# Kernel optimization log

Hardware: AMD Instinct MI355X
Metric: run time of the kernel (lower is better)

## Reference

```python
import jax, jax.numpy as jnp
import numpy as np

B, C, H, W = 4, 128, 64, 64


def setup_inputs() -> dict:
    key = jax.random.key(0)
    ks = jax.random.split(key, 4)
    x = jax.random.normal(ks[0], (B, C, H, W), dtype=jnp.float32)
    # 1x1 conv weights stored as [out_ch, in_ch]; biases [out_ch]
    Wf = jax.random.normal(ks[1], (1, C), dtype=jnp.float32) * 0.02
    bf = jnp.zeros((1,), dtype=jnp.float32)
    Wg = jax.random.normal(ks[2], (1, C), dtype=jnp.float32) * 0.02
    bg = jnp.zeros((1,), dtype=jnp.float32)
    Wh = jax.random.normal(ks[3], (C, C), dtype=jnp.float32) * 0.02
    bh = jnp.zeros((C,), dtype=jnp.float32)
    return {"x": x, "Wf": Wf, "bf": bf, "Wg": Wg, "bg": bg, "Wh": Wh, "bh": bh}


def reference(x, Wf, bf, Wg, bg, Wh, bh):
    b, c, h_, w_ = x.shape
    n = h_ * w_
    xf = x.reshape(b, c, n)  # [B, C, N]
    # 1x1 convs == per-pixel linear projections
    f = jnp.einsum('oc,bcn->bon', Wf, xf) + bf[None, :, None]  # [B, 1, N]
    g = jnp.einsum('oc,bcn->bon', Wg, xf) + bg[None, :, None]  # [B, 1, N]
    hh = jnp.einsum('oc,bcn->bon', Wh, xf) + bh[None, :, None]  # [B, C, N]
    # attention[b, i, j] = f[b, i] * g[b, j]; softmax over j (last dim)
    logits = jnp.einsum('bdi,bdj->bij', f, g)  # [B, N, N] (d=1)
    attn = jax.nn.softmax(logits, axis=-1)
    # bmm(h, attention): out[b, c, i] = sum_j h[b, c, j] * attn[b, j, i]
    sa = jnp.einsum('bcj,bji->bci', hh, attn)  # [B, C, N]
    return sa.reshape(b, c, h_, w_) + x
```

## Files before the change

kernel.cpp:

```cpp
#include <hip/hip_runtime.h>


#define B_ 4
#define C_ 128
#define N_ 4096
#define K_ 16

__device__ __forceinline__ float wave_reduce(float v) {
    #pragma unroll
    for (int off = 32; off > 0; off >>= 1) v += __shfl_down(v, off);
    return v;
}

__global__ __launch_bounds__(512) void kA(
    const float* __restrict__ x,
    const float* __restrict__ Wf, const float* __restrict__ bf,
    const float* __restrict__ Wg, const float* __restrict__ bg,
    float* __restrict__ f, float* __restrict__ g, float* __restrict__ Spart)
{
    int blk = blockIdx.x;
    int b   = blk >> 6;
    int n0  = (blk & 63) * 64;
    int tid = threadIdx.x, wave = tid >> 6, lane = tid & 63;

    const float* xb = x + (size_t)b * C_ * N_ + n0 + lane;
    float accf = 0.f, accg = 0.f;
    int cbeg = wave * 16;
    #pragma unroll
    for (int c = cbeg; c < cbeg + 16; ++c) {
        float xv = xb[(size_t)c * N_];
        accf += Wf[c] * xv;
        accg += Wg[c] * xv;
    }
    __shared__ float lf[8][64], lg[8][64];
    lf[wave][lane] = accf; lg[wave][lane] = accg;
    __syncthreads();
    if (tid < 64) {
        float s = 0.f;
        #pragma unroll
        for (int w2 = 0; w2 < 8; ++w2) s += lf[w2][tid];
        f[b * N_ + n0 + tid] = s + bf[0];
    } else if (tid < 128) {
        int l = lane;
        float s = 0.f;
        #pragma unroll
        for (int w2 = 0; w2 < 8; ++w2) s += lg[w2][l];
        float gv = s + bg[0];
        g[b * N_ + n0 + l] = gv;
        float p = 1.f;
        #pragma unroll
        for (int k = 0; k < K_; ++k) {
            float v = wave_reduce(p);
            if (l == 0) Spart[blk * K_ + k] = v;
            p *= gv;
        }
    }
}

__global__ __launch_bounds__(256) void kB(
    const float* __restrict__ x, const float* __restrict__ f,
    const float* __restrict__ Spart,
    float* __restrict__ Mt, float* __restrict__ t)
{
    static constexpr float INV_FACT[K_] = {
        1.f, 1.f, 0.5f, 1.6666667e-01f, 4.1666668e-02f, 8.3333338e-03f,
        1.3888889e-03f, 1.9841270e-04f, 2.4801587e-05f, 2.7557319e-06f,
        2.7557319e-07f, 2.5052108e-08f, 2.0876757e-09f, 1.6059044e-10f,
        1.1470746e-11f, 7.6471637e-13f };
    static constexpr float CK[K_] = {
        1.f, 0.5f, 3.3333334e-01f, 0.25f, 0.2f, 1.6666667e-01f,
        1.4285715e-01f, 0.125f, 1.1111111e-01f, 0.1f, 9.0909094e-02f,
        8.3333336e-02f, 7.6923079e-02f, 7.1428575e-02f, 6.6666670e-02f,
        6.25e-02f };

    int r   = blockIdx.x;
    int b   = r / (C_ + 1);
    int c   = r % (C_ + 1);
    int tid = threadIdx.x, wave = tid >> 6, lane = tid & 63;

    __shared__ float sred[16][16];
    __shared__ float Sfin[16];
    {
        int k = tid & 15, grp = tid >> 4;
        const float* Sp = Spart + (size_t)(b * 64 + grp * 4) * K_ + k;
        sred[grp][k] = Sp[0] + Sp[K_] + Sp[2 * K_] + Sp[3 * K_];
    }
    __syncthreads();
    if (tid < 16) {
        float s = 0.f;
        #pragma unroll
        for (int gi = 0; gi < 16; ++gi) s += sred[gi][tid];
        Sfin[tid] = s;
    }
    __syncthreads();
    float hk[K_];
    #pragma unroll
    for (int k = 0; k < K_; ++k) hk[k] = Sfin[k] * INV_FACT[k];

    const float* fb = f + b * N_;
    const float* xr = x + ((size_t)b * C_ + c) * N_;
    bool real = (c < C_);

    float acc[K_];
    #pragma unroll
    for (int k = 0; k < K_; ++k) acc[k] = 0.f;

    #pragma unroll
    for (int it = 0; it < 4; ++it) {
        int j = it * 1024 + tid * 4;
        float4 f4 = *(const float4*)(fb + j);
        float4 x4 = real ? *(const float4*)(xr + j) : make_float4(1.f, 1.f, 1.f, 1.f);
        float fe[4] = { f4.x, f4.y, f4.z, f4.w };
        float xe[4] = { x4.x, x4.y, x4.z, x4.w };
        #pragma unroll
        for (int e = 0; e < 4; ++e) {
            float fv = fe[e];
            float d = hk[K_ - 1];
            #pragma unroll
            for (int k = K_ - 2; k >= 0; --k) d = fmaf(d, fv, hk[k]);
            float u = xe[e] * __builtin_amdgcn_rcpf(d);
            #pragma unroll
            for (int k = 0; k < K_; ++k) {
                acc[k] += u;
                if (k < K_ - 1) u *= fv * CK[k];
            }
        }
    }

    #pragma unroll
    for (int k = 0; k < K_; ++k) acc[k] = wave_reduce(acc[k]);

    __shared__ float red[4][K_];
    if (lane == 0) {
        #pragma unroll
        for (int k = 0; k < K_; ++k) red[wave][k] = acc[k];
    }
    __syncthreads();
    if (tid < K_) {
        float v = red[0][tid] + red[1][tid] + red[2][tid] + red[3][tid];
        if (real) Mt[((size_t)b * K_ + tid) * C_ + c] = v;
        else      t[b * K_ + tid] = v;
    }
}

__global__ __launch_bounds__(256) void kD(
    const float* __restrict__ x, const float* __restrict__ g,
    const float* __restrict__ Wh, const float* __restrict__ bh,
    const float* __restrict__ Mt, const float* __restrict__ tvec,
    float* __restrict__ out)
{
    int row = blockIdx.x;
    int b   = row >> 7;
    int c   = row & 127;
    int tid = threadIdx.x;

    __shared__ float red[16][16];
    __shared__ float aK[K_];
    {
        int k = tid >> 4, ch = tid & 15;
        const float* Whp = Wh + (size_t)c * C_ + ch * 8;
        const float* Mtp = Mt + ((size_t)b * K_ + k) * C_ + ch * 8;
        float s = 0.f;
        #pragma unroll
        for (int i = 0; i < 8; ++i) s += Whp[i] * Mtp[i];
        red[k][ch] = s;
    }
    __syncthreads();
    if (tid < K_) {
        float s = 0.f;
        #pragma unroll
        for (int ch = 0; ch < 16; ++ch) s += red[tid][ch];
        aK[tid] = s + bh[c] * tvec[b * K_ + tid];
    }
    __syncthreads();
    float a[K_];
    #pragma unroll
    for (int k = 0; k < K_; ++k) a[k] = aK[k];

    const float* xr = x + (size_t)row * N_;
    const float* gb = g + (size_t)b * N_;
    float* orow = out + (size_t)row * N_;

    #pragma unroll
    for (int it = 0; it < 4; ++it) {
        int i = it * 1024 + tid * 4;
        float4 g4 = *(const float4*)(gb + i);
        float4 x4 = *(const float4*)(xr + i);
        float ge[4] = { g4.x, g4.y, g4.z, g4.w };
        float xe[4] = { x4.x, x4.y, x4.z, x4.w };
        float oe[4];
        #pragma unroll
        for (int e = 0; e < 4; ++e) {
            float r = a[K_ - 1];
            #pragma unroll
            for (int k = K_ - 2; k >= 0; --k) r = fmaf(r, ge[e], a[k]);
            oe[e] = xe[e] + r;
        }
        float4 o4 = { oe[0], oe[1], oe[2], oe[3] };
        *(float4*)(orow + i) = o4;
    }
}

extern "C" void kernel_launch(void* const* d_in, const int* in_sizes, int n_in,
                              void* d_out, int out_size, void* d_ws, size_t ws_size,
                              hipStream_t stream)
{
    const float* x  = (const float*)d_in[0];
    const float* Wf = (const float*)d_in[1];
    const float* bf = (const float*)d_in[2];
    const float* Wg = (const float*)d_in[3];
    const float* bg = (const float*)d_in[4];
    const float* Wh = (const float*)d_in[5];
    const float* bh = (const float*)d_in[6];
    float* out = (float*)d_out;

    float* ws    = (float*)d_ws;
    const int BN = B_ * N_;
    float* f     = ws;
    float* g     = ws + BN;
    float* Spart = ws + 2 * BN;
    float* Mt    = Spart + 256 * K_;
    float* t     = Mt + B_ * K_ * C_;

    kA<<<256, 512, 0, stream>>>(x, Wf, bf, Wg, bg, f, g, Spart);
    kB<<<B_ * (C_ + 1), 256, 0, stream>>>(x, f, Spart, Mt, t);
    kD<<<B_ * C_, 256, 0, stream>>>(x, g, Wh, bh, Mt, t, out);
}
```

Baseline: 22.74 us.

## Fuse three kernels into one cooperative persistent kernel with grid syncs

Replaces the three separate launches (projection, moment accumulation, output) with a single cooperative kernel of 256 blocks of 512 threads, using grid.sync between phases. Each block now loops over several rows per phase, and the Spart reduction is done once for all batches per block. This is meant to remove inter-kernel launch gaps and tail effects. The cost is grid-wide barrier overhead, the cooperative launch path, and reduced parallelism in the later phases: 256 blocks each handle two or three rows serially instead of launching 516 or 512 blocks.

```diff
diff --git a/kernel.cpp b/kernel.cpp
--- a/kernel.cpp
+++ b/kernel.cpp
@@ -1,4 +1,7 @@
 #include <hip/hip_runtime.h>
+#include <hip/hip_cooperative_groups.h>
+
+namespace cg = cooperative_groups;
 
 
 #define B_ 4
@@ -12,55 +15,14 @@
     return v;
 }
 
-__global__ __launch_bounds__(512) void kA(
+__global__ __launch_bounds__(512, 1) void fused(
     const float* __restrict__ x,
     const float* __restrict__ Wf, const float* __restrict__ bf,
     const float* __restrict__ Wg, const float* __restrict__ bg,
-    float* __restrict__ f, float* __restrict__ g, float* __restrict__ Spart)
-{
-    int blk = blockIdx.x;
-    int b   = blk >> 6;
-    int n0  = (blk & 63) * 64;
-    int tid = threadIdx.x, wave = tid >> 6, lane = tid & 63;
-
-    const float* xb = x + (size_t)b * C_ * N_ + n0 + lane;
-    float accf = 0.f, accg = 0.f;
-    int cbeg = wave * 16;
-    #pragma unroll
-    for (int c = cbeg; c < cbeg + 16; ++c) {
-        float xv = xb[(size_t)c * N_];
-        accf += Wf[c] * xv;
-        accg += Wg[c] * xv;
-    }
-    __shared__ float lf[8][64], lg[8][64];
-    lf[wave][lane] = accf; lg[wave][lane] = accg;
-    __syncthreads();
-    if (tid < 64) {
-        float s = 0.f;
-        #pragma unroll
-        for (int w2 = 0; w2 < 8; ++w2) s += lf[w2][tid];
-        f[b * N_ + n0 + tid] = s + bf[0];
-    } else if (tid < 128) {
-        int l = lane;
-        float s = 0.f;
-        #pragma unroll
-        for (int w2 = 0; w2 < 8; ++w2) s += lg[w2][l];
-        float gv = s + bg[0];
-        g[b * N_ + n0 + l] = gv;
-        float p = 1.f;
-        #pragma unroll
-        for (int k = 0; k < K_; ++k) {
-            float v = wave_reduce(p);
-            if (l == 0) Spart[blk * K_ + k] = v;
-            p *= gv;
-        }
-    }
-}
-
-__global__ __launch_bounds__(256) void kB(
-    const float* __restrict__ x, const float* __restrict__ f,
-    const float* __restrict__ Spart,
-    float* __restrict__ Mt, float* __restrict__ t)
+    const float* __restrict__ Wh, const float* __restrict__ bh,
+    float* __restrict__ f, float* __restrict__ g,
+    float* __restrict__ Spart, float* __restrict__ Mt,
+    float* __restrict__ tvec, float* __restrict__ out)
 {
     static constexpr float INV_FACT[K_] = {
         1.f, 1.f, 0.5f, 1.6666667e-01f, 4.1666668e-02f, 8.3333338e-03f,
@@ -73,131 +35,176 @@
         8.3333336e-02f, 7.6923079e-02f, 7.1428575e-02f, 6.6666670e-02f,
         6.25e-02f };
 
-    int r   = blockIdx.x;
-    int b   = r / (C_ + 1);
-    int c   = r % (C_ + 1);
-    int tid = threadIdx.x, wave = tid >> 6, lane = tid & 63;
-
-    __shared__ float sred[16][16];
-    __shared__ float Sfin[16];
+    cg::grid_group grid = cg::this_grid();
+    const int blk  = blockIdx.x;
+    const int tid  = threadIdx.x;
+    const int wave = tid >> 6, lane = tid & 63;
+
+    __shared__ float lf[8][64];
+    __shared__ float lg[8][64];
+    __shared__ float sred[4][K_][4];
+    __shared__ float Sh[4][K_];
+    __shared__ float red2[8][K_];
+    __shared__ float red3[K_][16];
+    __shared__ float aK[K_];
+
     {
-        int k = tid & 15, grp = tid >> 4;
-        const float* Sp = Spart + (size_t)(b * 64 + grp * 4) * K_ + k;
-        sred[grp][k] = Sp[0] + Sp[K_] + Sp[2 * K_] + Sp[3 * K_];
+        int b  = blk >> 6;
+        int n0 = (blk & 63) * 64;
+        const float* xb = x + (size_t)b * C_ * N_ + n0 + lane;
+        float accf = 0.f, accg = 0.f;
+        int cbeg = wave * 16;
+        #pragma unroll
+        for (int c = cbeg; c < cbeg + 16; ++c) {
+            float xv = xb[(size_t)c * N_];
+            accf += Wf[c] * xv;
+            accg += Wg[c] * xv;
+        }
+        lf[wave][lane] = accf; lg[wave][lane] = accg;
+        __syncthreads();
+        if (tid < 64) {
+            float s = 0.f;
+            #pragma unroll
+            for (int w2 = 0; w2 < 8; ++w2) s += lf[w2][tid];
+            f[b * N_ + n0 + tid] = s + bf[0];
+        } else if (tid < 128) {
+            int l = lane;
+            float s = 0.f;
+            #pragma unroll
+            for (int w2 = 0; w2 < 8; ++w2) s += lg[w2][l];
+            float gv = s + bg[0];
+            g[b * N_ + n0 + l] = gv;
+            float p = 1.f;
+            #pragma unroll
+            for (int k = 0; k < K_; ++k) {
+                float v = wave_reduce(p);
+                if (l == 0) Spart[blk * K_ + k] = v;
+                p *= gv;
+            }
+        }
+    }
+    grid.sync();
+
+    if (tid < 256) {
+        int b = tid >> 6, k = (tid >> 2) & 15, grp = tid & 3;
+        const float* Sp = Spart + (size_t)(b * 64 + grp * 16) * K_ + k;
+        float s = 0.f;
+        #pragma unroll
+        for (int p = 0; p < 16; ++p) s += Sp[p * K_];
+        sred[b][k][grp] = s;
     }
     __syncthreads();
-    if (tid < 16) {
-        float s = 0.f;
-        #pragma unroll
-        for (int gi = 0; gi < 16; ++gi) s += sred[gi][tid];
-        Sfin[tid] = s;
+    if (tid < 64) {
+        int b = tid >> 4, k = tid & 15;
+        Sh[b][k] = (sred[b][k][0] + sred[b][k][1] + sred[b][k][2] + sred[b][k][3])
+                   * INV_FACT[k];
     }
     __syncthreads();
-    float hk[K_];
-    #pragma unroll
-    for (int k = 0; k < K_; ++k) hk[k] = Sfin[k] * INV_FACT[k];
-
-    const float* fb = f + b * N_;
-    const float* xr = x + ((size_t)b * C_ + c) * N_;
-    bool real = (c < C_);
-
-    float acc[K_];
-    #pragma unroll
-    for (int k = 0; k < K_; ++k) acc[k] = 0.f;
-
-    #pragma unroll
-    for (int it = 0; it < 4; ++it) {
-        int j = it * 1024 + tid * 4;
-        float4 f4 = *(const float4*)(fb + j);
-        float4 x4 = real ? *(const float4*)(xr + j) : make_float4(1.f, 1.f, 1.f, 1.f);
-        float fe[4] = { f4.x, f4.y, f4.z, f4.w };
-        float xe[4] = { x4.x, x4.y, x4.z, x4.w };
-        #pragma unroll
-        for (int e = 0; e < 4; ++e) {
-            float fv = fe[e];
-            float d = hk[K_ - 1];
-            #pragma unroll
-            for (int k = K_ - 2; k >= 0; --k) d = fmaf(d, fv, hk[k]);
-            float u = xe[e] * __builtin_amdgcn_rcpf(d);
-            #pragma unroll
-            for (int k = 0; k < K_; ++k) {
-                acc[k] += u;
-                if (k < K_ - 1) u *= fv * CK[k];
+
+    for (int r = blk; r < B_ * (C_ + 1); r += 256) {
+        int b = r / (C_ + 1);
+        int c = r % (C_ + 1);
+        bool real = (c < C_);
+        const float* fb = f + b * N_;
+        const float* xr = x + ((size_t)b * C_ + c) * N_;
+
+        float hk[K_];
+        #pragma unroll
+        for (int k = 0; k < K_; ++k) hk[k] = Sh[b][k];
+
+        float acc[K_];
+        #pragma unroll
+        for (int k = 0; k < K_; ++k) acc[k] = 0.f;
+
+        #pragma unroll
+        for (int it = 0; it < 2; ++it) {
+            int j = it * 2048 + tid * 4;
+            float4 f4 = *(const float4*)(fb + j);
+            float4 x4 = real ? *(const float4*)(xr + j)
+                             : make_float4(1.f, 1.f, 1.f, 1.f);
+            float fe[4] = { f4.x, f4.y, f4.z, f4.w };
+            float xe[4] = { x4.x, x4.y, x4.z, x4.w };
+            #pragma unroll
+            for (int e = 0; e < 4; ++e) {
+                float fv = fe[e];
+                float d = hk[K_ - 1];
+                #pragma unroll
+                for (int k = K_ - 2; k >= 0; --k) d = fmaf(d, fv, hk[k]);
+                float u = xe[e] * __builtin_amdgcn_rcpf(d);
+                #pragma unroll
+                for (int k = 0; k < K_; ++k) {
+                    acc[k] += u;
+                    if (k < K_ - 1) u *= fv * CK[k];
+                }
             }
         }
-    }
-
-    #pragma unroll
-    for (int k = 0; k < K_; ++k) acc[k] = wave_reduce(acc[k]);
-
-    __shared__ float red[4][K_];
-    if (lane == 0) {
-        #pragma unroll
-        for (int k = 0; k < K_; ++k) red[wave][k] = acc[k];
-    }
-    __syncthreads();
-    if (tid < K_) {
-        float v = red[0][tid] + red[1][tid] + red[2][tid] + red[3][tid];
-        if (real) Mt[((size_t)b * K_ + tid) * C_ + c] = v;
-        else      t[b * K_ + tid] = v;
-    }
-}
-
-__global__ __launch_bounds__(256) void kD(
-    const float* __restrict__ x, const float* __restrict__ g,
-    const float* __restrict__ Wh, const float* __restrict__ bh,
-    const float* __restrict__ Mt, const float* __restrict__ tvec,
-    float* __restrict__ out)
-{
-    int row = blockIdx.x;
-    int b   = row >> 7;
-    int c   = row & 127;
-    int tid = threadIdx.x;
-
-    __shared__ float red[16][16];
-    __shared__ float aK[K_];
-    {
-        int k = tid >> 4, ch = tid & 15;
-        const float* Whp = Wh + (size_t)c * C_ + ch * 8;
-        const float* Mtp = Mt + ((size_t)b * K_ + k) * C_ + ch * 8;
-        float s = 0.f;
-        #pragma unroll
-        for (int i = 0; i < 8; ++i) s += Whp[i] * Mtp[i];
-        red[k][ch] = s;
-    }
-    __syncthreads();
-    if (tid < K_) {
-        float s = 0.f;
-        #pragma unroll
-        for (int ch = 0; ch < 16; ++ch) s += red[tid][ch];
-        aK[tid] = s + bh[c] * tvec[b * K_ + tid];
-    }
-    __syncthreads();
-    float a[K_];
-    #pragma unroll
-    for (int k = 0; k < K_; ++k) a[k] = aK[k];
-
-    const float* xr = x + (size_t)row * N_;
-    const float* gb = g + (size_t)b * N_;
-    float* orow = out + (size_t)row * N_;
-
-    #pragma unroll
-    for (int it = 0; it < 4; ++it) {
-        int i = it * 1024 + tid * 4;
-        float4 g4 = *(const float4*)(gb + i);
-        float4 x4 = *(const float4*)(xr + i);
-        float ge[4] = { g4.x, g4.y, g4.z, g4.w };
-        float xe[4] = { x4.x, x4.y, x4.z, x4.w };
-        float oe[4];
-        #pragma unroll
-        for (int e = 0; e < 4; ++e) {
-            float r = a[K_ - 1];
-            #pragma unroll
-            for (int k = K_ - 2; k >= 0; --k) r = fmaf(r, ge[e], a[k]);
-            oe[e] = xe[e] + r;
-        }
-        float4 o4 = { oe[0], oe[1], oe[2], oe[3] };
-        *(float4*)(orow + i) = o4;
+
+        #pragma unroll
+        for (int k = 0; k < K_; ++k) acc[k] = wave_reduce(acc[k]);
+        if (lane == 0) {
+            #pragma unroll
+            for (int k = 0; k < K_; ++k) red2[wave][k] = acc[k];
+        }
+        __syncthreads();
+        if (tid < K_) {
+            float v = 0.f;
+            #pragma unroll
+            for (int w2 = 0; w2 < 8; ++w2) v += red2[w2][tid];
+            if (real) Mt[((size_t)b * K_ + tid) * C_ + c] = v;
+            else      tvec[b * K_ + tid] = v;
+        }
+        __syncthreads();
+    }
+    grid.sync();
+
+    for (int row = blk; row < B_ * C_; row += 256) {
+        int b = row >> 7;
+        int c = row & 127;
+
+        if (tid < 256) {
+            int k = tid >> 4, ch = tid & 15;
+            const float* Whp = Wh + (size_t)c * C_ + ch * 8;
+            const float* Mtp = Mt + ((size_t)b * K_ + k) * C_ + ch * 8;
+            float s = 0.f;
+            #pragma unroll
+            for (int i = 0; i < 8; ++i) s += Whp[i] * Mtp[i];
+            red3[k][ch] = s;
+        }
+        __syncthreads();
+        if (tid < K_) {
+            float s = 0.f;
+            #pragma unroll
+            for (int ch = 0; ch < 16; ++ch) s += red3[tid][ch];
+            aK[tid] = s + bh[c] * tvec[b * K_ + tid];
+        }
+        __syncthreads();
+        float a[K_];
+        #pragma unroll
+        for (int k = 0; k < K_; ++k) a[k] = aK[k];
+
+        const float* xr = x + (size_t)row * N_;
+        const float* gb = g + (size_t)b * N_;
+        float* orow = out + (size_t)row * N_;
+
+        #pragma unroll
+        for (int it = 0; it < 2; ++it) {
+            int i = it * 2048 + tid * 4;
+            float4 g4 = *(const float4*)(gb + i);
+            float4 x4 = *(const float4*)(xr + i);
+            float ge[4] = { g4.x, g4.y, g4.z, g4.w };
+            float xe[4] = { x4.x, x4.y, x4.z, x4.w };
+            float oe[4];
+            #pragma unroll
+            for (int e = 0; e < 4; ++e) {
+                float rr = a[K_ - 1];
+                #pragma unroll
+                for (int k = K_ - 2; k >= 0; --k) rr = fmaf(rr, ge[e], a[k]);
+                oe[e] = xe[e] + rr;
+            }
+            float4 o4 = { oe[0], oe[1], oe[2], oe[3] };
+            *(float4*)(orow + i) = o4;
+        }
+        __syncthreads();
     }
 }
 
@@ -220,9 +227,10 @@
     float* g     = ws + BN;
     float* Spart = ws + 2 * BN;
     float* Mt    = Spart + 256 * K_;
-    float* t     = Mt + B_ * K_ * C_;
-
-    kA<<<256, 512, 0, stream>>>(x, Wf, bf, Wg, bg, f, g, Spart);
-    kB<<<B_ * (C_ + 1), 256, 0, stream>>>(x, f, Spart, Mt, t);
-    kD<<<B_ * C_, 256, 0, stream>>>(x, g, Wh, bh, Mt, t, out);
+    float* tvec  = Mt + (size_t)B_ * K_ * C_;
+
+    void* args[] = { (void*)&x, (void*)&Wf, (void*)&bf, (void*)&Wg, (void*)&bg,
+                     (void*)&Wh, (void*)&bh, (void*)&f, (void*)&g,
+                     (void*)&Spart, (void*)&Mt, (void*)&tvec, (void*)&out };
+    hipLaunchCooperativeKernel((void*)fused, dim3(256), dim3(512), args, 0, stream);
 }
```

After: 83.19 us. 3.66x slower.
